# Performance work log

Hardware: AMD Instinct MI355X
Metric: run time of the kernel (lower is better)

The kernel has to match this reference:

```python
import jax, jax.numpy as jnp
import numpy as np

T, K, E, H, I = 2048, 8, 32, 1024, 768


def setup_inputs() -> dict:
    key = jax.random.key(0)
    k0, k1, k2, k3, k4, k5 = jax.random.split(key, 6)
    sh = 1.0 / np.sqrt(H).astype(np.float32)
    si = 1.0 / np.sqrt(I).astype(np.float32)
    return {
        "hidden_states": jax.random.normal(k0, (T, H), jnp.float32),
        "top_k_index": jax.random.randint(k1, (T, K), 0, E),
        "top_k_weights": jax.random.uniform(k2, (T, K), jnp.float32),
        "gate_proj": jax.random.normal(k3, (E, I, H), jnp.float32) * sh,
        "up_proj": jax.random.normal(k4, (E, I, H), jnp.float32) * sh,
        "down_proj": jax.random.normal(k5, (E, H, I), jnp.float32) * si,
    }


def reference(hidden_states, top_k_index, top_k_weights, gate_proj, up_proj, down_proj):
    # Tokens not routed to expert e get combine weight 0, so summing the
    # weighted per-expert outputs over all experts reproduces the original
    # gather -> SwiGLU MLP -> scale -> index_add_ exactly (duplicated expert
    # hits within a token's top-k sum, matching repeated index_add_).
    n_tok = hidden_states.shape[0]
    n_exp = gate_proj.shape[0]
    combine = jnp.zeros((n_tok, n_exp), hidden_states.dtype)
    combine = combine.at[jnp.arange(n_tok)[:, None], top_k_index].add(top_k_weights)

    def body(acc, xs):
        g_w, u_w, d_w, w_e = xs  # g_w,u_w: [I,H]; d_w: [H,I]; w_e: [T]
        h = jax.nn.silu(hidden_states @ g_w.T) * (hidden_states @ u_w.T)  # [T,I]
        y = h @ d_w.T  # [T,H]
        return acc + y * w_e[:, None], None

    out, _ = jax.lax.scan(
        body,
        jnp.zeros_like(hidden_states),
        (gate_proj, up_proj, down_proj, combine.T),
    )
    return out
```

## Files before the change

kernel.cpp:

```cpp
#include <hip/hip_runtime.h>

#define T_TOK 2048
#define TOPK  8
#define NEXP  32
#define HDIM  1024
#define IDIM  768
#define NPAIR (T_TOK * TOPK)
#define BM 128
#define BK 32
#define MT_MAX (NPAIR / BM + NEXP)

typedef __attribute__((ext_vector_type(8))) short short8;
typedef __attribute__((ext_vector_type(4))) float f32x4;

__device__ __forceinline__ unsigned short f2bf(float f) {
    unsigned x = __float_as_uint(f);
    unsigned r = x + 0x7fffu + ((x >> 16) & 1u);
    return (unsigned short)(r >> 16);
}
__device__ __forceinline__ float bf2f(unsigned short u) {
    return __uint_as_float(((unsigned)u) << 16);
}

__device__ __forceinline__ void gl_lds16(const unsigned short* g, void* l) {
    __builtin_amdgcn_global_load_lds((const __attribute__((address_space(1))) void*)g,
                                     (__attribute__((address_space(3))) void*)l, 16, 0, 0);
}

__global__ void k_conv2(const float* __restrict__ src0, const float* __restrict__ src1,
                        unsigned short* __restrict__ dst, int n4each) {
    int i = blockIdx.x * 256 + threadIdx.x;
    const float* s = (i < n4each) ? src0 : src1;
    int j = (i < n4each) ? i : i - n4each;
    if (i < 2 * n4each) {
        float4 v = ((const float4*)s)[j];
        ushort4 o;
        o.x = f2bf(v.x); o.y = f2bf(v.y); o.z = f2bf(v.z); o.w = f2bf(v.w);
        ((ushort4*)dst)[i] = o;
    }
}

__global__ void k_conv(const float* __restrict__ src, unsigned short* __restrict__ dst, int n4) {
    int i = blockIdx.x * 256 + threadIdx.x;
    if (i < n4) {
        float4 v = ((const float4*)src)[i];
        ushort4 o;
        o.x = f2bf(v.x); o.y = f2bf(v.y); o.z = f2bf(v.z); o.w = f2bf(v.w);
        ((ushort4*)dst)[i] = o;
    }
}

__global__ void k_init(int* counts) {
    if (threadIdx.x < NEXP) counts[threadIdx.x] = 0;
}

__global__ void k_hist(const int* __restrict__ idx, int* __restrict__ counts) {
    int p = blockIdx.x * 256 + threadIdx.x;
    atomicAdd(&counts[idx[p]], 1);
}

__global__ void k_scan(const int* __restrict__ counts, int* __restrict__ offsets,
                       int* __restrict__ mtb, int* __restrict__ cursor) {
    if (threadIdx.x == 0) {
        int tot = 0, mt = 0;
        for (int e = 0; e < NEXP; ++e) {
            offsets[e] = tot; mtb[e] = mt;
            tot += counts[e];
            mt += (counts[e] + BM - 1) / BM;
        }
        offsets[NEXP] = tot; mtb[NEXP] = mt;
    }
    if (threadIdx.x < NEXP) cursor[threadIdx.x] = 0;
}

__global__ void k_scatter(const int* __restrict__ idx, int* __restrict__ cursor,
                          const int* __restrict__ offsets, int* __restrict__ pair_token,
                          int* __restrict__ pair_slot) {
    int p = blockIdx.x * 256 + threadIdx.x;
    int e = idx[p];
    int pos = atomicAdd(&cursor[e], 1);
    int slot = offsets[e] + pos;
    pair_token[slot] = p >> 3;
    pair_slot[p] = slot;
}

__global__ __launch_bounds__(256, 2) void k_gateup(
    const unsigned short* __restrict__ hid_bf, const unsigned short* __restrict__ gate_bf,
    const unsigned short* __restrict__ up_bf, const int* __restrict__ pair_token,
    const int* __restrict__ offsets, const int* __restrict__ mtb,
    unsigned short* __restrict__ h_mid)
{
    __shared__ short8 sA[512], sBg[512], sBu[512];
    __shared__ int sInfo[4];
    int tid = threadIdx.x;
    if (tid == 0) {
        int mt = blockIdx.x;
        if (mt >= mtb[NEXP]) { sInfo[0] = -1; }
        else {
            int e = 0;
            while (mtb[e + 1] <= mt) e++;
            sInfo[0] = e; sInfo[1] = offsets[e];
            sInfo[2] = offsets[e + 1] - offsets[e];
            sInfo[3] = (mt - mtb[e]) * BM;
        }
    }
    __syncthreads();
    int e = sInfo[0];
    if (e < 0) return;
    int off = sInfo[1], Me = sInfo[2], mrow0 = sInfo[3];
    int n0 = blockIdx.y * 128;

    int wave = tid >> 6, lane = tid & 63, quad = lane >> 4, l16 = lane & 15;

    int m0 = wave * 32 + l16, m1 = m0 + 16;
    int rp0 = mrow0 + m0, rp1 = mrow0 + m1;
    int tok0 = (rp0 < Me) ? pair_token[off + rp0] : 0;
    int tok1 = (rp1 < Me) ? pair_token[off + rp1] : 0;
    const unsigned short* aG0 = hid_bf + (size_t)tok0 * HDIM + quad * 8;
    const unsigned short* aG1 = hid_bf + (size_t)tok1 * HDIM + quad * 8;
    const unsigned short* gG0 = gate_bf + ((size_t)e * IDIM + n0 + m0) * HDIM + quad * 8;
    const unsigned short* gG1 = gate_bf + ((size_t)e * IDIM + n0 + m1) * HDIM + quad * 8;
    const unsigned short* uG0 = up_bf + ((size_t)e * IDIM + n0 + m0) * HDIM + quad * 8;
    const unsigned short* uG1 = up_bf + ((size_t)e * IDIM + n0 + m1) * HDIM + quad * 8;
    void* ldsA0 = (void*)&sA[wave * 128];  void* ldsA1 = (void*)&sA[wave * 128 + 64];
    void* ldsG0 = (void*)&sBg[wave * 128]; void* ldsG1 = (void*)&sBg[wave * 128 + 64];
    void* ldsU0 = (void*)&sBu[wave * 128]; void* ldsU1 = (void*)&sBu[wave * 128 + 64];

    int wm = (wave & 1) * 64, wn = (wave >> 1) * 64;
    int aBase = (wm >> 4) * 64 + quad * 16 + l16;
    int bBase = (wn >> 4) * 64 + quad * 16 + l16;

    f32x4 zero = {0.f, 0.f, 0.f, 0.f};
    f32x4 accg[4][4], accu[4][4];
#pragma unroll
    for (int i = 0; i < 4; ++i)
#pragma unroll
        for (int j = 0; j < 4; ++j) { accg[i][j] = zero; accu[i][j] = zero; }

    for (int k0 = 0; k0 < HDIM; k0 += BK) {
        gl_lds16(aG0 + k0, ldsA0); gl_lds16(aG1 + k0, ldsA1);
        gl_lds16(gG0 + k0, ldsG0); gl_lds16(gG1 + k0, ldsG1);
        gl_lds16(uG0 + k0, ldsU0); gl_lds16(uG1 + k0, ldsU1);
        __syncthreads();
        short8 af[4];
#pragma unroll
        for (int fm = 0; fm < 4; ++fm) af[fm] = sA[aBase + fm * 64];
#pragma unroll
        for (int fn = 0; fn < 4; ++fn) {
            short8 bg = sBg[bBase + fn * 64];
            short8 bu = sBu[bBase + fn * 64];
#pragma unroll
            for (int fm = 0; fm < 4; ++fm) {
                accg[fm][fn] = __builtin_amdgcn_mfma_f32_16x16x32_bf16(af[fm], bg, accg[fm][fn], 0, 0, 0);
                accu[fm][fn] = __builtin_amdgcn_mfma_f32_16x16x32_bf16(af[fm], bu, accu[fm][fn], 0, 0, 0);
            }
        }
        __syncthreads();
    }

#pragma unroll
    for (int fm = 0; fm < 4; ++fm)
#pragma unroll
        for (int fn = 0; fn < 4; ++fn)
#pragma unroll
            for (int r = 0; r < 4; ++r) {
                int mloc = wm + fm * 16 + quad * 4 + r;
                int prow = mrow0 + mloc;
                if (prow < Me) {
                    int col = n0 + wn + fn * 16 + l16;
                    float g = accg[fm][fn][r], u = accu[fm][fn][r];
                    float h = g / (1.f + __expf(-g)) * u;
                    h_mid[(size_t)(off + prow) * IDIM + col] = f2bf(h);
                }
            }
}

__global__ __launch_bounds__(256, 2) void k_down(
    const unsigned short* __restrict__ h_mid, const unsigned short* __restrict__ down_bf,
    const int* __restrict__ offsets, const int* __restrict__ mtb,
    unsigned short* __restrict__ y_pair)
{
    __shared__ short8 sA[512], sB[1024];
    __shared__ int sInfo[4];
    int tid = threadIdx.x;
    if (tid == 0) {
        int mt = blockIdx.x;
        if (mt >= mtb[NEXP]) { sInfo[0] = -1; }
        else {
            int e = 0;
            while (mtb[e + 1] <= mt) e++;
            sInfo[0] = e; sInfo[1] = offsets[e];
            sInfo[2] = offsets[e + 1] - offsets[e];
            sInfo[3] = (mt - mtb[e]) * BM;
        }
    }
    __syncthreads();
    int e = sInfo[0];
    if (e < 0) return;
    int off = sInfo[1], Me = sInfo[2], mrow0 = sInfo[3];
    int n0 = blockIdx.y * 256;

    int wave = tid >> 6, lane = tid & 63, quad = lane >> 4, l16 = lane & 15;

    int m0 = wave * 32 + l16, m1 = m0 + 16;
    int rp0 = mrow0 + m0; if (rp0 >= Me) rp0 = 0;
    int rp1 = mrow0 + m1; if (rp1 >= Me) rp1 = 0;
    const unsigned short* aG0 = h_mid + (size_t)(off + rp0) * IDIM + quad * 8;
    const unsigned short* aG1 = h_mid + (size_t)(off + rp1) * IDIM + quad * 8;
    const unsigned short* bG0 = down_bf + ((size_t)e * HDIM + n0 + wave * 64 + l16) * IDIM + quad * 8;
    const unsigned short* bG1 = bG0 + (size_t)16 * IDIM;
    const unsigned short* bG2 = bG0 + (size_t)32 * IDIM;
    const unsigned short* bG3 = bG0 + (size_t)48 * IDIM;
    void* ldsA0 = (void*)&sA[wave * 128];      void* ldsA1 = (void*)&sA[wave * 128 + 64];
    void* ldsB0 = (void*)&sB[wave * 256];      void* ldsB1 = (void*)&sB[wave * 256 + 64];
    void* ldsB2 = (void*)&sB[wave * 256 + 128]; void* ldsB3 = (void*)&sB[wave * 256 + 192];

    int wm = (wave & 1) * 64, wn = (wave >> 1) * 128;
    int aBase = (wm >> 4) * 64 + quad * 16 + l16;
    int bBase = (wn >> 4) * 64 + quad * 16 + l16;

    f32x4 zero = {0.f, 0.f, 0.f, 0.f};
    f32x4 acc[4][8];
#pragma unroll
    for (int i = 0; i < 4; ++i)
#pragma unroll
        for (int j = 0; j < 8; ++j) acc[i][j] = zero;

    for (int k0 = 0; k0 < IDIM; k0 += BK) {
        gl_lds16(aG0 + k0, ldsA0); gl_lds16(aG1 + k0, ldsA1);
        gl_lds16(bG0 + k0, ldsB0); gl_lds16(bG1 + k0, ldsB1);
        gl_lds16(bG2 + k0, ldsB2); gl_lds16(bG3 + k0, ldsB3);
        __syncthreads();
        short8 af[4];
#pragma unroll
        for (int fm = 0; fm < 4; ++fm) af[fm] = sA[aBase + fm * 64];
#pragma unroll
        for (int fn = 0; fn < 8; ++fn) {
            short8 bf = sB[bBase + fn * 64];
#pragma unroll
            for (int fm = 0; fm < 4; ++fm)
                acc[fm][fn] = __builtin_amdgcn_mfma_f32_16x16x32_bf16(af[fm], bf, acc[fm][fn], 0, 0, 0);
        }
        __syncthreads();
    }

#pragma unroll
    for (int fm = 0; fm < 4; ++fm)
#pragma unroll
        for (int fn = 0; fn < 8; ++fn)
#pragma unroll
            for (int r = 0; r < 4; ++r) {
                int mloc = wm + fm * 16 + quad * 4 + r;
                int prow = mrow0 + mloc;
                if (prow < Me) {
                    int col = n0 + wn + fn * 16 + l16;
                    y_pair[(size_t)(off + prow) * HDIM + col] = f2bf(acc[fm][fn][r]);
                }
            }
}

__global__ void k_reduce(const unsigned short* __restrict__ y_pair,
                         const int* __restrict__ pair_slot,
                         const float* __restrict__ topw, float* __restrict__ out)
{
    int t = blockIdx.x;
    __shared__ int ss[TOPK];
    __shared__ float sw[TOPK];
    if (threadIdx.x < TOPK) {
        ss[threadIdx.x] = pair_slot[t * TOPK + threadIdx.x];
        sw[threadIdx.x] = topw[t * TOPK + threadIdx.x];
    }
    __syncthreads();
    int c = threadIdx.x * 4;
    float a0 = 0.f, a1 = 0.f, a2 = 0.f, a3 = 0.f;
    for (int k = 0; k < TOPK; ++k) {
        const unsigned short* yr = y_pair + (size_t)ss[k] * HDIM + c;
        uint2 v = *(const uint2*)yr;
        float w = sw[k];
        a0 += w * bf2f((unsigned short)(v.x & 0xffff));
        a1 += w * bf2f((unsigned short)(v.x >> 16));
        a2 += w * bf2f((unsigned short)(v.y & 0xffff));
        a3 += w * bf2f((unsigned short)(v.y >> 16));
    }
    float4 o = {a0, a1, a2, a3};
    *(float4*)(out + (size_t)t * HDIM + c) = o;
}

extern "C" void kernel_launch(void* const* d_in, const int* in_sizes, int n_in,
                              void* d_out, int out_size, void* d_ws, size_t ws_size,
                              hipStream_t stream) {
    (void)in_sizes; (void)n_in; (void)out_size; (void)ws_size;
    const float* hidden = (const float*)d_in[0];
    const int*   tki    = (const int*)d_in[1];
    const float* tkw    = (const float*)d_in[2];
    const float* gate   = (const float*)d_in[3];
    const float* up     = (const float*)d_in[4];
    const float* down   = (const float*)d_in[5];
    float* out = (float*)d_out;

    char* w = (char*)d_ws;
    unsigned short* h_mid   = (unsigned short*)w;
    unsigned short* hid_bf  = (unsigned short*)(w + 25165824);
    unsigned short* gate_bf = (unsigned short*)(w + 29360128);
    unsigned short* up_bf   = (unsigned short*)(w + 79691776);
    unsigned short* down_bf = gate_bf;
    unsigned short* y_pair  = up_bf;
    int* ib = (int*)(w + 130023424);
    int* pair_token = ib;
    int* pair_slot  = ib + NPAIR;
    int* counts     = ib + 2 * NPAIR;
    int* cursor     = counts + NEXP;
    int* offsets    = cursor + NEXP;
    int* mtb        = offsets + NEXP + 1;

    const int W4 = NEXP * IDIM * HDIM / 4;
    const int H4 = T_TOK * HDIM / 4;

    k_init<<<1, 64, 0, stream>>>(counts);
    k_hist<<<NPAIR / 256, 256, 0, stream>>>(tki, counts);
    k_scan<<<1, 64, 0, stream>>>(counts, offsets, mtb, cursor);
    k_scatter<<<NPAIR / 256, 256, 0, stream>>>(tki, cursor, offsets, pair_token, pair_slot);

    k_conv<<<(H4 + 255) / 256, 256, 0, stream>>>(hidden, hid_bf, H4);
    k_conv2<<<(2 * W4 + 255) / 256, 256, 0, stream>>>(gate, up, gate_bf, W4);

    k_gateup<<<dim3(MT_MAX, IDIM / 128), 256, 0, stream>>>(hid_bf, gate_bf, up_bf,
                                                           pair_token, offsets, mtb, h_mid);

    k_conv<<<(W4 + 255) / 256, 256, 0, stream>>>(down, down_bf, W4);

    k_down<<<dim3(MT_MAX, HDIM / 256), 256, 0, stream>>>(h_mid, down_bf, offsets, mtb, y_pair);
    k_reduce<<<T_TOK, 256, 0, stream>>>(y_pair, pair_slot, tkw, out);
}
```

Measured before the change: 558.8 us.

## Schedule expert tiles onto XCDs via load-balanced table and double BK

Adds a scheduling table, built in the scan kernel, that assigns each (M-tile, N-column) work item of gate/up and down to one of 8 XCD slots using greedy least-loaded placement per expert. Block IDs are interleaved modulo 8, so all blocks of an expert's column land on the same XCD and share its L2 for weight reuse. It also doubles the K tile to 64 with a new LDS layout, halving the barrier count per tile. The cost is more LDS per block, possibly lowering occupancy, extra padding blocks that exit early, and a serial single-thread table build.

Measured after the change: 715.1 us. +28.0%, slower.

```diff
diff --git a/kernel.cpp b/kernel.cpp
--- a/kernel.cpp
+++ b/kernel.cpp
@@ -7,8 +7,11 @@
 #define IDIM  768
 #define NPAIR (T_TOK * TOPK)
 #define BM 128
-#define BK 32
-#define MT_MAX (NPAIR / BM + NEXP)
+#define BK 64
+#define NYG (IDIM / 128)
+#define NYD (HDIM / 256)
+#define GU_CAP 384
+#define DN_CAP 256
 
 typedef __attribute__((ext_vector_type(8))) short short8;
 typedef __attribute__((ext_vector_type(4))) float f32x4;
@@ -60,8 +63,14 @@
 }
 
 __global__ void k_scan(const int* __restrict__ counts, int* __restrict__ offsets,
-                       int* __restrict__ mtb, int* __restrict__ cursor) {
-    if (threadIdx.x == 0) {
+                       int* __restrict__ mtb, int* __restrict__ cursor,
+                       int* __restrict__ wg_tab, int* __restrict__ wd_tab) {
+    int tid = threadIdx.x;
+    for (int i = tid; i < 8 * GU_CAP; i += 64) wg_tab[i] = -1;
+    for (int i = tid; i < 8 * DN_CAP; i += 64) wd_tab[i] = -1;
+    if (tid < NEXP) cursor[tid] = 0;
+    __syncthreads();
+    if (tid == 0) {
         int tot = 0, mt = 0;
         for (int e = 0; e < NEXP; ++e) {
             offsets[e] = tot; mtb[e] = mt;
@@ -69,8 +78,22 @@
             mt += (counts[e] + BM - 1) / BM;
         }
         offsets[NEXP] = tot; mtb[NEXP] = mt;
-    }
-    if (threadIdx.x < NEXP) cursor[threadIdx.x] = 0;
+        int loadg[8], loadd[8];
+        for (int x = 0; x < 8; ++x) { loadg[x] = 0; loadd[x] = 0; }
+        for (int e = 0; e < NEXP; ++e) {
+            int t0 = mtb[e], t1 = mtb[e + 1];
+            for (int y = 0; y < NYG; ++y) {
+                int x = 0;
+                for (int j = 1; j < 8; ++j) if (loadg[j] < loadg[x]) x = j;
+                for (int t = t0; t < t1; ++t) wg_tab[x * GU_CAP + loadg[x]++] = (t << 3) | y;
+            }
+            for (int y = 0; y < NYD; ++y) {
+                int x = 0;
+                for (int j = 1; j < 8; ++j) if (loadd[j] < loadd[x]) x = j;
+                for (int t = t0; t < t1; ++t) wd_tab[x * DN_CAP + loadd[x]++] = (t << 3) | y;
+            }
+        }
+    }
 }
 
 __global__ void k_scatter(const int* __restrict__ idx, int* __restrict__ cursor,
@@ -88,27 +111,29 @@
     const unsigned short* __restrict__ hid_bf, const unsigned short* __restrict__ gate_bf,
     const unsigned short* __restrict__ up_bf, const int* __restrict__ pair_token,
     const int* __restrict__ offsets, const int* __restrict__ mtb,
-    unsigned short* __restrict__ h_mid)
+    const int* __restrict__ wg_tab, unsigned short* __restrict__ h_mid)
 {
-    __shared__ short8 sA[512], sBg[512], sBu[512];
-    __shared__ int sInfo[4];
+    __shared__ short8 sA[1024], sBg[1024], sBu[1024];
+    __shared__ int sInfo[5];
     int tid = threadIdx.x;
     if (tid == 0) {
-        int mt = blockIdx.x;
-        if (mt >= mtb[NEXP]) { sInfo[0] = -1; }
+        int bx = blockIdx.x;
+        int w = wg_tab[(bx & 7) * GU_CAP + (bx >> 3)];
+        if (w < 0) { sInfo[0] = -1; }
         else {
+            int mt = w >> 3, y = w & 7;
             int e = 0;
             while (mtb[e + 1] <= mt) e++;
             sInfo[0] = e; sInfo[1] = offsets[e];
             sInfo[2] = offsets[e + 1] - offsets[e];
             sInfo[3] = (mt - mtb[e]) * BM;
+            sInfo[4] = y * 128;
         }
     }
     __syncthreads();
     int e = sInfo[0];
     if (e < 0) return;
-    int off = sInfo[1], Me = sInfo[2], mrow0 = sInfo[3];
-    int n0 = blockIdx.y * 128;
+    int off = sInfo[1], Me = sInfo[2], mrow0 = sInfo[3], n0 = sInfo[4];
 
     int wave = tid >> 6, lane = tid & 63, quad = lane >> 4, l16 = lane & 15;
 
@@ -122,13 +147,9 @@
     const unsigned short* gG1 = gate_bf + ((size_t)e * IDIM + n0 + m1) * HDIM + quad * 8;
     const unsigned short* uG0 = up_bf + ((size_t)e * IDIM + n0 + m0) * HDIM + quad * 8;
     const unsigned short* uG1 = up_bf + ((size_t)e * IDIM + n0 + m1) * HDIM + quad * 8;
-    void* ldsA0 = (void*)&sA[wave * 128];  void* ldsA1 = (void*)&sA[wave * 128 + 64];
-    void* ldsG0 = (void*)&sBg[wave * 128]; void* ldsG1 = (void*)&sBg[wave * 128 + 64];
-    void* ldsU0 = (void*)&sBu[wave * 128]; void* ldsU1 = (void*)&sBu[wave * 128 + 64];
+    int c00 = (2 * wave) * 8 * 16, c10 = (2 * wave + 1) * 8 * 16;
 
     int wm = (wave & 1) * 64, wn = (wave >> 1) * 64;
-    int aBase = (wm >> 4) * 64 + quad * 16 + l16;
-    int bBase = (wn >> 4) * 64 + quad * 16 + l16;
 
     f32x4 zero = {0.f, 0.f, 0.f, 0.f};
     f32x4 accg[4][4], accu[4][4];
@@ -138,21 +159,29 @@
         for (int j = 0; j < 4; ++j) { accg[i][j] = zero; accu[i][j] = zero; }
 
     for (int k0 = 0; k0 < HDIM; k0 += BK) {
-        gl_lds16(aG0 + k0, ldsA0); gl_lds16(aG1 + k0, ldsA1);
-        gl_lds16(gG0 + k0, ldsG0); gl_lds16(gG1 + k0, ldsG1);
-        gl_lds16(uG0 + k0, ldsU0); gl_lds16(uG1 + k0, ldsU1);
+        gl_lds16(aG0 + k0,      &sA[c00]);      gl_lds16(aG0 + k0 + 32, &sA[c00 + 64]);
+        gl_lds16(aG1 + k0,      &sA[c10]);      gl_lds16(aG1 + k0 + 32, &sA[c10 + 64]);
+        gl_lds16(gG0 + k0,      &sBg[c00]);     gl_lds16(gG0 + k0 + 32, &sBg[c00 + 64]);
+        gl_lds16(gG1 + k0,      &sBg[c10]);     gl_lds16(gG1 + k0 + 32, &sBg[c10 + 64]);
+        gl_lds16(uG0 + k0,      &sBu[c00]);     gl_lds16(uG0 + k0 + 32, &sBu[c00 + 64]);
+        gl_lds16(uG1 + k0,      &sBu[c10]);     gl_lds16(uG1 + k0 + 32, &sBu[c10 + 64]);
         __syncthreads();
-        short8 af[4];
-#pragma unroll
-        for (int fm = 0; fm < 4; ++fm) af[fm] = sA[aBase + fm * 64];
-#pragma unroll
-        for (int fn = 0; fn < 4; ++fn) {
-            short8 bg = sBg[bBase + fn * 64];
-            short8 bu = sBu[bBase + fn * 64];
-#pragma unroll
-            for (int fm = 0; fm < 4; ++fm) {
-                accg[fm][fn] = __builtin_amdgcn_mfma_f32_16x16x32_bf16(af[fm], bg, accg[fm][fn], 0, 0, 0);
-                accu[fm][fn] = __builtin_amdgcn_mfma_f32_16x16x32_bf16(af[fm], bu, accu[fm][fn], 0, 0, 0);
+#pragma unroll
+        for (int s = 0; s < 2; ++s) {
+            int aB = ((wm >> 4) * 8 + s * 4 + quad) * 16 + l16;
+            int bB = ((wn >> 4) * 8 + s * 4 + quad) * 16 + l16;
+            short8 af[4];
+#pragma unroll
+            for (int fm = 0; fm < 4; ++fm) af[fm] = sA[aB + fm * 128];
+#pragma unroll
+            for (int fn = 0; fn < 4; ++fn) {
+                short8 bg = sBg[bB + fn * 128];
+                short8 bu = sBu[bB + fn * 128];
+#pragma unroll
+                for (int fm = 0; fm < 4; ++fm) {
+                    accg[fm][fn] = __builtin_amdgcn_mfma_f32_16x16x32_bf16(af[fm], bg, accg[fm][fn], 0, 0, 0);
+                    accu[fm][fn] = __builtin_amdgcn_mfma_f32_16x16x32_bf16(af[fm], bu, accu[fm][fn], 0, 0, 0);
+                }
             }
         }
         __syncthreads();
@@ -178,27 +207,29 @@
 __global__ __launch_bounds__(256, 2) void k_down(
     const unsigned short* __restrict__ h_mid, const unsigned short* __restrict__ down_bf,
     const int* __restrict__ offsets, const int* __restrict__ mtb,
-    unsigned short* __restrict__ y_pair)
+    const int* __restrict__ wd_tab, unsigned short* __restrict__ y_pair)
 {
-    __shared__ short8 sA[512], sB[1024];
-    __shared__ int sInfo[4];
+    __shared__ short8 sA[1024], sB[2048];
+    __shared__ int sInfo[5];
     int tid = threadIdx.x;
     if (tid == 0) {
-        int mt = blockIdx.x;
-        if (mt >= mtb[NEXP]) { sInfo[0] = -1; }
+        int bx = blockIdx.x;
+        int w = wd_tab[(bx & 7) * DN_CAP + (bx >> 3)];
+        if (w < 0) { sInfo[0] = -1; }
         else {
+            int mt = w >> 3, y = w & 7;
             int e = 0;
             while (mtb[e + 1] <= mt) e++;
             sInfo[0] = e; sInfo[1] = offsets[e];
             sInfo[2] = offsets[e + 1] - offsets[e];
             sInfo[3] = (mt - mtb[e]) * BM;
+            sInfo[4] = y * 256;
         }
     }
     __syncthreads();
     int e = sInfo[0];
     if (e < 0) return;
-    int off = sInfo[1], Me = sInfo[2], mrow0 = sInfo[3];
-    int n0 = blockIdx.y * 256;
+    int off = sInfo[1], Me = sInfo[2], mrow0 = sInfo[3], n0 = sInfo[4];
 
     int wave = tid >> 6, lane = tid & 63, quad = lane >> 4, l16 = lane & 15;
 
@@ -211,13 +242,10 @@
     const unsigned short* bG1 = bG0 + (size_t)16 * IDIM;
     const unsigned short* bG2 = bG0 + (size_t)32 * IDIM;
     const unsigned short* bG3 = bG0 + (size_t)48 * IDIM;
-    void* ldsA0 = (void*)&sA[wave * 128];      void* ldsA1 = (void*)&sA[wave * 128 + 64];
-    void* ldsB0 = (void*)&sB[wave * 256];      void* ldsB1 = (void*)&sB[wave * 256 + 64];
-    void* ldsB2 = (void*)&sB[wave * 256 + 128]; void* ldsB3 = (void*)&sB[wave * 256 + 192];
+    int cA0 = (2 * wave) * 128, cA1 = (2 * wave + 1) * 128;
+    int cB0 = (4 * wave) * 128, cB1 = cB0 + 128, cB2 = cB0 + 256, cB3 = cB0 + 384;
 
     int wm = (wave & 1) * 64, wn = (wave >> 1) * 128;
-    int aBase = (wm >> 4) * 64 + quad * 16 + l16;
-    int bBase = (wn >> 4) * 64 + quad * 16 + l16;
 
     f32x4 zero = {0.f, 0.f, 0.f, 0.f};
     f32x4 acc[4][8];
@@ -227,19 +255,27 @@
         for (int j = 0; j < 8; ++j) acc[i][j] = zero;
 
     for (int k0 = 0; k0 < IDIM; k0 += BK) {
-        gl_lds16(aG0 + k0, ldsA0); gl_lds16(aG1 + k0, ldsA1);
-        gl_lds16(bG0 + k0, ldsB0); gl_lds16(bG1 + k0, ldsB1);
-        gl_lds16(bG2 + k0, ldsB2); gl_lds16(bG3 + k0, ldsB3);
+        gl_lds16(aG0 + k0, &sA[cA0]); gl_lds16(aG0 + k0 + 32, &sA[cA0 + 64]);
+        gl_lds16(aG1 + k0, &sA[cA1]); gl_lds16(aG1 + k0 + 32, &sA[cA1 + 64]);
+        gl_lds16(bG0 + k0, &sB[cB0]); gl_lds16(bG0 + k0 + 32, &sB[cB0 + 64]);
+        gl_lds16(bG1 + k0, &sB[cB1]); gl_lds16(bG1 + k0 + 32, &sB[cB1 + 64]);
+        gl_lds16(bG2 + k0, &sB[cB2]); gl_lds16(bG2 + k0 + 32, &sB[cB2 + 64]);
+        gl_lds16(bG3 + k0, &sB[cB3]); gl_lds16(bG3 + k0 + 32, &sB[cB3 + 64]);
         __syncthreads();
-        short8 af[4];
-#pragma unroll
-        for (int fm = 0; fm < 4; ++fm) af[fm] = sA[aBase + fm * 64];
-#pragma unroll
-        for (int fn = 0; fn < 8; ++fn) {
-            short8 bf = sB[bBase + fn * 64];
-#pragma unroll
-            for (int fm = 0; fm < 4; ++fm)
-                acc[fm][fn] = __builtin_amdgcn_mfma_f32_16x16x32_bf16(af[fm], bf, acc[fm][fn], 0, 0, 0);
+#pragma unroll
+        for (int s = 0; s < 2; ++s) {
+            int aB = ((wm >> 4) * 8 + s * 4 + quad) * 16 + l16;
+            int bB = ((wn >> 4) * 8 + s * 4 + quad) * 16 + l16;
+            short8 af[4];
+#pragma unroll
+            for (int fm = 0; fm < 4; ++fm) af[fm] = sA[aB + fm * 128];
+#pragma unroll
+            for (int fn = 0; fn < 8; ++fn) {
+                short8 bf = sB[bB + fn * 128];
+#pragma unroll
+                for (int fm = 0; fm < 4; ++fm)
+                    acc[fm][fn] = __builtin_amdgcn_mfma_f32_16x16x32_bf16(af[fm], bf, acc[fm][fn], 0, 0, 0);
+            }
         }
         __syncthreads();
     }
@@ -312,23 +348,25 @@
     int* cursor     = counts + NEXP;
     int* offsets    = cursor + NEXP;
     int* mtb        = offsets + NEXP + 1;
+    int* wg_tab     = mtb + NEXP + 1;
+    int* wd_tab     = wg_tab + 8 * GU_CAP;
 
     const int W4 = NEXP * IDIM * HDIM / 4;
     const int H4 = T_TOK * HDIM / 4;
 
     k_init<<<1, 64, 0, stream>>>(counts);
     k_hist<<<NPAIR / 256, 256, 0, stream>>>(tki, counts);
-    k_scan<<<1, 64, 0, stream>>>(counts, offsets, mtb, cursor);
+    k_scan<<<1, 64, 0, stream>>>(counts, offsets, mtb, cursor, wg_tab, wd_tab);
     k_scatter<<<NPAIR / 256, 256, 0, stream>>>(tki, cursor, offsets, pair_token, pair_slot);
 
     k_conv<<<(H4 + 255) / 256, 256, 0, stream>>>(hidden, hid_bf, H4);
     k_conv2<<<(2 * W4 + 255) / 256, 256, 0, stream>>>(gate, up, gate_bf, W4);
 
-    k_gateup<<<dim3(MT_MAX, IDIM / 128), 256, 0, stream>>>(hid_bf, gate_bf, up_bf,
-                                                           pair_token, offsets, mtb, h_mid);
+    k_gateup<<<8 * GU_CAP, 256, 0, stream>>>(hid_bf, gate_bf, up_bf,
+                                             pair_token, offsets, mtb, wg_tab, h_mid);
 
     k_conv<<<(W4 + 255) / 256, 256, 0, stream>>>(down, down_bf, W4);
 
-    k_down<<<dim3(MT_MAX, HDIM / 256), 256, 0, stream>>>(h_mid, down_bf, offsets, mtb, y_pair);
+    k_down<<<8 * DN_CAP, 256, 0, stream>>>(h_mid, down_bf, offsets, mtb, wd_tab, y_pair);
     k_reduce<<<T_TOK, 256, 0, stream>>>(y_pair, pair_slot, tkw, out);
 }
```
